# Performance work log

Measured on AMD Instinct MI355X. Metric: run time of the kernel, lower is better.

The kernel has to match this reference:

```python
import jax, jax.numpy as jnp
import numpy as np

B, T, C = 8, 1024, 1024
EPS = 1e-5
NEG_INF = -1e38


def layernorm(x, w, b):
    mu = jnp.mean(x, axis=-1, keepdims=True)
    var = jnp.var(x, axis=-1, keepdims=True)
    return (x - mu) * jax.lax.rsqrt(var + EPS) * w + b


def wkv_scan(w, u, k, v):
    """Numerically-stable RWKV-4 WKV recurrence (forward direction).
    w: [C] (negative decay), u: [C] bonus, k, v: [B, T, C]. Returns [B, T, C]."""
    kt = jnp.swapaxes(k, 0, 1)  # [T, B, C]
    vt = jnp.swapaxes(v, 0, 1)
    bsz = k.shape[0]
    a0 = jnp.zeros((bsz, C), k.dtype)
    b0 = jnp.zeros((bsz, C), k.dtype)
    p0 = jnp.full((bsz, C), NEG_INF, k.dtype)

    def step(carry, inp):
        a, b, p = carry
        kk, vv = inp
        # output at current step (with bonus u on current token)
        q = jnp.maximum(p, u + kk)
        e1 = jnp.exp(p - q)
        e2 = jnp.exp(u + kk - q)
        out = (e1 * a + e2 * vv) / (e1 * b + e2)
        # decay state and absorb current token
        q2 = jnp.maximum(p + w, kk)
        f1 = jnp.exp(p + w - q2)
        f2 = jnp.exp(kk - q2)
        return (f1 * a + f2 * vv, f1 * b + f2, q2), out

    _, outs = jax.lax.scan(step, (a0, b0, p0), (kt, vt))
    return jnp.swapaxes(outs, 0, 1)  # [B, T, C]


def setup_inputs() -> dict:
    key = jax.random.key(0)
    ks = jax.random.split(key, 12)
    s = 0.02
    d = {}
    d["x"] = jax.random.normal(ks[0], (B, T, C), jnp.float32)
    d["ln1_w"] = jnp.ones((C,), jnp.float32)
    d["ln1_b"] = jnp.zeros((C,), jnp.float32)
    d["ln2_w"] = jnp.ones((C,), jnp.float32)
    d["ln2_b"] = jnp.zeros((C,), jnp.float32)
    d["Wr"] = jax.random.normal(ks[1], (C, C), jnp.float32) * s
    d["Wk"] = jax.random.normal(ks[2], (C, C), jnp.float32) * s
    d["Wv"] = jax.random.normal(ks[3], (C, C), jnp.float32) * s
    d["Wo"] = jax.random.normal(ks[4], (C, C), jnp.float32) * s
    d["decay"] = jax.random.normal(ks[5], (C,), jnp.float32) * 0.1
    d["u"] = jax.random.normal(ks[6], (C,), jnp.float32) * 0.1
    d["Wfk"] = jax.random.normal(ks[7], (4 * C, C), jnp.float32) * s
    d["Wfv"] = jax.random.normal(ks[8], (C, 4 * C), jnp.float32) * s
    d["Wfr"] = jax.random.normal(ks[9], (C, C), jnp.float32) * s
    return d


def reference(x, ln1_w, ln1_b, ln2_w, ln2_b, Wr, Wk, Wv, Wo, decay, u, Wfk, Wfv, Wfr):
    # --- bidirectional time-mix (WKV attention) ---
    xn = layernorm(x, ln1_w, ln1_b)
    r = jax.nn.sigmoid(xn @ Wr.T)
    k = xn @ Wk.T
    v = xn @ Wv.T
    w = -jnp.exp(decay)  # per-channel negative decay
    wkv_f = wkv_scan(w, u, k, v)
    wkv_b = jnp.flip(wkv_scan(w, u, jnp.flip(k, axis=1), jnp.flip(v, axis=1)), axis=1)
    wkv = 0.5 * (wkv_f + wkv_b)
    x = x + (r * wkv) @ Wo.T
    # --- channel-mix FFN ---
    xn2 = layernorm(x, ln2_w, ln2_b)
    kk = jnp.square(jax.nn.relu(xn2 @ Wfk.T))  # [B, T, 4C]
    x = x + jax.nn.sigmoid(xn2 @ Wfr.T) * (kk @ Wfv.T)
    return x
```

## Files before the change

### kernel.cpp

```cpp
#include <hip/hip_runtime.h>
#include <cstdint>
#include <cstddef>

typedef unsigned short u16;
typedef __bf16 bf16_t;
typedef bf16_t bf16x8 __attribute__((ext_vector_type(8)));
typedef float f32x4 __attribute__((ext_vector_type(4)));

#define GCH 16
#define TCH 64

static __device__ __forceinline__ float bf2f(u16 v) {
    union { unsigned int u; float f; } cv;
    cv.u = ((unsigned int)v) << 16;
    return cv.f;
}
static __device__ __forceinline__ u16 f2bf(float f) {
    union { float f; unsigned int u; } cv;
    cv.f = f;
    unsigned int r = 0x7fffu + ((cv.u >> 16) & 1u);
    return (u16)((cv.u + r) >> 16);
}

__global__ __launch_bounds__(256)
void f2bf_kernel(const float* __restrict__ in, u16* __restrict__ out, int n4)
{
    const int i = blockIdx.x * 256 + threadIdx.x;
    if (i < n4) {
        float4 f = ((const float4*)in)[i];
        ushort4 o;
        o.x = f2bf(f.x); o.y = f2bf(f.y); o.z = f2bf(f.z); o.w = f2bf(f.w);
        ((ushort4*)out)[i] = o;
    }
}

__global__ __launch_bounds__(256)
void ln_kernel(const float* __restrict__ xin, const float* __restrict__ w,
               const float* __restrict__ b, u16* __restrict__ out)
{
    const int row = blockIdx.x;
    const int tid = threadIdx.x;
    const float4 f = ((const float4*)(xin + (size_t)row * 1024))[tid];
    float vals[4] = { f.x, f.y, f.z, f.w };
    float s  = vals[0] + vals[1] + vals[2] + vals[3];
    float ss = vals[0]*vals[0] + vals[1]*vals[1] + vals[2]*vals[2] + vals[3]*vals[3];
    for (int off = 32; off; off >>= 1) {
        s  += __shfl_down(s, off, 64);
        ss += __shfl_down(ss, off, 64);
    }
    __shared__ float redS[4], redQ[4];
    if ((tid & 63) == 0) { redS[tid >> 6] = s; redQ[tid >> 6] = ss; }
    __syncthreads();
    s  = redS[0] + redS[1] + redS[2] + redS[3];
    ss = redQ[0] + redQ[1] + redQ[2] + redQ[3];
    const float mu  = s * (1.f / 1024.f);
    const float var = ss * (1.f / 1024.f) - mu * mu;
    const float rs  = rsqrtf(var + 1e-5f);
    const float4 wv = ((const float4*)w)[tid];
    const float4 bv = ((const float4*)b)[tid];
    ushort4 o;
    o.x = f2bf((vals[0] - mu) * rs * wv.x + bv.x);
    o.y = f2bf((vals[1] - mu) * rs * wv.y + bv.y);
    o.z = f2bf((vals[2] - mu) * rs * wv.z + bv.z);
    o.w = f2bf((vals[3] - mu) * rs * wv.w + bv.w);
    ((ushort4*)(out + (size_t)row * 1024))[tid] = o;
}

template<int EPI>
__global__ __launch_bounds__(256)
void gemm_bt(const u16* __restrict__ A, const u16* __restrict__ B,
             int M, int N, int K,
             void* __restrict__ outp,
             const void* __restrict__ aux1, const void* __restrict__ aux2)
{
    __shared__ u16 lA[128 * 64];
    __shared__ u16 lB[128 * 64];
    const int tid  = threadIdx.x;
    const int wave = tid >> 6;
    const int lane = tid & 63;
    const int q    = lane >> 4;
    const int l16  = lane & 15;
    const long mBase = (long)blockIdx.x * 128;
    const long nBase = (long)blockIdx.y * 128;
    const int wm = (wave >> 1) * 64;
    const int wn = (wave & 1) * 64;

    f32x4 acc[4][4];
#pragma unroll
    for (int i = 0; i < 4; ++i)
#pragma unroll
        for (int j = 0; j < 4; ++j)
#pragma unroll
            for (int r = 0; r < 4; ++r) acc[i][j][r] = 0.f;

    const int srow = tid >> 3;
    const int scol = ((tid & 7) ^ (srow & 7)) * 8;
    const int ldsW = wave * 512;
    const int swz = l16 & 7;

    for (int kb = 0; kb < K; kb += 64) {
        __syncthreads();
#pragma unroll
        for (int c = 0; c < 4; ++c) {
            const int row = c * 32 + srow;
            const u16* ga = A + (mBase + row) * (long)K + kb + scol;
            const u16* gb = B + (nBase + row) * (long)K + kb + scol;
            __builtin_amdgcn_global_load_lds(
                (const __attribute__((address_space(1))) void*)ga,
                (__attribute__((address_space(3))) void*)(lA + c * 2048 + ldsW),
                16, 0, 0);
            __builtin_amdgcn_global_load_lds(
                (const __attribute__((address_space(1))) void*)gb,
                (__attribute__((address_space(3))) void*)(lB + c * 2048 + ldsW),
                16, 0, 0);
        }
        __syncthreads();
#pragma unroll
        for (int ks = 0; ks < 2; ++ks) {
            const int grp = ((ks * 4 + q) ^ swz) * 8;
            bf16x8 af[4], bfm[4];
#pragma unroll
            for (int i = 0; i < 4; ++i) {
                af[i]  = *(const bf16x8*)(lA + (wm + i * 16 + l16) * 64 + grp);
                bfm[i] = *(const bf16x8*)(lB + (wn + i * 16 + l16) * 64 + grp);
            }
#pragma unroll
            for (int i = 0; i < 4; ++i)
#pragma unroll
                for (int j = 0; j < 4; ++j)
                    acc[i][j] = __builtin_amdgcn_mfma_f32_16x16x32_bf16(
                        af[i], bfm[j], acc[i][j], 0, 0, 0);
        }
    }

    if (EPI == 5 || EPI == 6) {
        u16* optr; long sN, cb;
        if (EPI == 5) {
            const long seg = nBase >> 10;
            optr = (u16*)(seg == 0 ? outp
                        : seg == 1 ? (void*)aux1 : (void*)aux2);
            sN = 1024; cb = (nBase & 1023) + wn + l16;
        } else {
            if (nBase < 4096) { optr = (u16*)outp; sN = 4096; cb = nBase + wn + l16; }
            else { optr = (u16*)aux1; sN = 1024; cb = (nBase - 4096) + wn + l16; }
        }
#pragma unroll
        for (int i = 0; i < 4; ++i)
#pragma unroll
            for (int r = 0; r < 4; ++r) {
                const long row = mBase + wm + i * 16 + q * 4 + r;
                const long rowOff = row * sN + cb;
#pragma unroll
                for (int j = 0; j < 4; ++j) {
                    const float val = acc[i][j][r];
                    float t;
                    if (EPI == 5) t = val;
                    else if (nBase < 4096) t = val > 0.f ? val * val : 0.f;
                    else t = __fdividef(1.f, 1.f + __expf(-val));
                    optr[rowOff + j * 16] = f2bf(t);
                }
            }
    } else {
        const long colBase = nBase + wn + l16;
#pragma unroll
        for (int i = 0; i < 4; ++i) {
#pragma unroll
            for (int r = 0; r < 4; ++r) {
                const long row = mBase + wm + i * 16 + q * 4 + r;
                const long rowOff = row * (long)N;
#pragma unroll
                for (int j = 0; j < 4; ++j) {
                    const long idx = rowOff + colBase + j * 16;
                    const float val = acc[i][j][r];
                    if (EPI == 0) {
                        ((u16*)outp)[idx] = f2bf(val);
                    } else if (EPI == 1) {
                        ((float*)outp)[idx] = ((const float*)aux1)[idx] + val;
                    } else if (EPI == 2) {
                        const float t = val > 0.f ? val * val : 0.f;
                        ((u16*)outp)[idx] = f2bf(t);
                    } else if (EPI == 3) {
                        const float sg = __fdividef(1.f, 1.f + __expf(-val));
                        ((u16*)outp)[idx] = f2bf(sg);
                    } else {
                        const float t = ((const float*)aux1)[idx]
                                      + bf2f(((const u16*)aux2)[idx]) * val;
                        ((float*)outp)[idx] = t;
                    }
                }
            }
        }
    }
}

__global__ __launch_bounds__(64)
void wkv_sum(const u16* __restrict__ kbuf, const u16* __restrict__ vbuf,
             const float* __restrict__ decay,
             float* __restrict__ sumA, float* __restrict__ sumB,
             float* __restrict__ sumP)
{
    const int c   = blockIdx.x * 64 + threadIdx.x;
    const int bt  = blockIdx.y;
    const int dir = blockIdx.z & 1;
    const int g   = blockIdx.z >> 1;
    const long base = (long)bt * (1024 * 1024) + c;
    const long stride = dir ? -1024 : 1024;
    long idx = dir ? base + (long)(1023 - g * TCH) * 1024
                   : base + (long)(g * TCH) * 1024;
    const float w = -__expf(decay[c]);
    float a = 0.f, b = 0.f, p = -1e38f;

    float kq[8], vq[8];
#pragma unroll
    for (int j = 0; j < 8; ++j) {
        kq[j] = bf2f(kbuf[idx + j * stride]);
        vq[j] = bf2f(vbuf[idx + j * stride]);
    }
    for (int tb = 0; tb < TCH / 8; ++tb) {
        float kn[8], vn[8];
        if (tb < TCH / 8 - 1) {
#pragma unroll
            for (int j = 0; j < 8; ++j) {
                kn[j] = bf2f(kbuf[idx + (j + 8) * stride]);
                vn[j] = bf2f(vbuf[idx + (j + 8) * stride]);
            }
        }
#pragma unroll
        for (int j = 0; j < 8; ++j) {
            const float kk = kq[j], vv = vq[j];
            const float pw = p + w;
            const float q2 = fmaxf(pw, kk);
            const float f1 = __expf(pw - q2);
            const float f2 = __expf(kk - q2);
            a = f1 * a + f2 * vv;
            b = f1 * b + f2;
            p = q2;
        }
#pragma unroll
        for (int j = 0; j < 8; ++j) { kq[j] = kn[j]; vq[j] = vn[j]; }
        idx += 8 * stride;
    }
    const int sidx = (((dir * GCH + g) * 8 + bt) << 10) + c;
    sumA[sidx] = a; sumB[sidx] = b; sumP[sidx] = p;
}

__global__ __launch_bounds__(64)
void wkv_out(const u16* __restrict__ kbuf, const u16* __restrict__ vbuf,
             const float* __restrict__ decay, const float* __restrict__ uarr,
             const float* __restrict__ sumA, const float* __restrict__ sumB,
             const float* __restrict__ sumP,
             u16* __restrict__ wkvf, u16* __restrict__ wkvb)
{
    const int c   = blockIdx.x * 64 + threadIdx.x;
    const int bt  = blockIdx.y;
    const int dir = blockIdx.z & 1;
    const int g   = blockIdx.z >> 1;
    const long base = (long)bt * (1024 * 1024) + c;
    const long stride = dir ? -1024 : 1024;
    long idx = dir ? base + (long)(1023 - g * TCH) * 1024
                   : base + (long)(g * TCH) * 1024;
    u16* __restrict__ dst = dir ? wkvb : wkvf;

    const float w  = -__expf(decay[c]);
    const float uu = uarr[c];
    float a = 0.f, b = 0.f, p = -1e38f;
    for (int gg = 0; gg < g; ++gg) {
        const int sidx = (((dir * GCH + gg) * 8 + bt) << 10) + c;
        const float a2 = sumA[sidx], b2 = sumB[sidx], p2 = sumP[sidx];
        const float pd = p + w * (float)TCH;
        const float qq = fmaxf(pd, p2);
        const float x1 = __expf(pd - qq);
        const float x2 = __expf(p2 - qq);
        a = x1 * a + x2 * a2;
        b = x1 * b + x2 * b2;
        p = qq;
    }

    float kq[8], vq[8];
#pragma unroll
    for (int j = 0; j < 8; ++j) {
        kq[j] = bf2f(kbuf[idx + j * stride]);
        vq[j] = bf2f(vbuf[idx + j * stride]);
    }
    for (int tb = 0; tb < TCH / 8; ++tb) {
        float kn[8], vn[8];
        if (tb < TCH / 8 - 1) {
#pragma unroll
            for (int j = 0; j < 8; ++j) {
                kn[j] = bf2f(kbuf[idx + (j + 8) * stride]);
                vn[j] = bf2f(vbuf[idx + (j + 8) * stride]);
            }
        }
#pragma unroll
        for (int j = 0; j < 8; ++j) {
            const float kk = kq[j], vv = vq[j];
            const float uk = uu + kk;
            const float q1 = fmaxf(p, uk);
            const float e1 = __expf(p - q1);
            const float e2 = __expf(uk - q1);
            dst[idx + j * stride] = f2bf(__fdividef(e1 * a + e2 * vv, e1 * b + e2));
            const float pw = p + w;
            const float q2 = fmaxf(pw, kk);
            const float f1 = __expf(pw - q2);
            const float f2 = __expf(kk - q2);
            a = f1 * a + f2 * vv;
            b = f1 * b + f2;
            p = q2;
        }
#pragma unroll
        for (int j = 0; j < 8; ++j) { kq[j] = kn[j]; vq[j] = vn[j]; }
        idx += 8 * stride;
    }
}

__global__ __launch_bounds__(256)
void combine_kernel(u16* __restrict__ wkvf, const u16* __restrict__ wkvb,
                    const u16* __restrict__ rpre)
{
    const int i = blockIdx.x * 256 + threadIdx.x;
    ushort4 fv = ((const ushort4*)wkvf)[i];
    ushort4 bv = ((const ushort4*)wkvb)[i];
    ushort4 rv = ((const ushort4*)rpre)[i];
    ushort4 o;
    {
        float r0 = __fdividef(1.f, 1.f + __expf(-bf2f(rv.x)));
        float r1 = __fdividef(1.f, 1.f + __expf(-bf2f(rv.y)));
        float r2 = __fdividef(1.f, 1.f + __expf(-bf2f(rv.z)));
        float r3 = __fdividef(1.f, 1.f + __expf(-bf2f(rv.w)));
        o.x = f2bf(r0 * 0.5f * (bf2f(fv.x) + bf2f(bv.x)));
        o.y = f2bf(r1 * 0.5f * (bf2f(fv.y) + bf2f(bv.y)));
        o.z = f2bf(r2 * 0.5f * (bf2f(fv.z) + bf2f(bv.z)));
        o.w = f2bf(r3 * 0.5f * (bf2f(fv.w) + bf2f(bv.w)));
    }
    ((ushort4*)wkvf)[i] = o;
}

extern "C" void kernel_launch(void* const* d_in, const int* in_sizes, int n_in,
                              void* d_out, int out_size, void* d_ws, size_t ws_size,
                              hipStream_t stream)
{
    (void)in_sizes; (void)n_in; (void)out_size; (void)ws_size;
    const float* x     = (const float*)d_in[0];
    const float* ln1w  = (const float*)d_in[1];
    const float* ln1b  = (const float*)d_in[2];
    const float* ln2w  = (const float*)d_in[3];
    const float* ln2b  = (const float*)d_in[4];
    const float* Wr    = (const float*)d_in[5];
    const float* Wk    = (const float*)d_in[6];
    const float* Wv    = (const float*)d_in[7];
    const float* Wo    = (const float*)d_in[8];
    const float* decay = (const float*)d_in[9];
    const float* uarr  = (const float*)d_in[10];
    const float* Wfk   = (const float*)d_in[11];
    const float* Wfv   = (const float*)d_in[12];
    const float* Wfr   = (const float*)d_in[13];

    const int M = 8192, C = 1024, C4 = 4096;
    const size_t MB = 1024u * 1024u;
    char* ws = (char*)d_ws;
    float* X2   = (float*)(ws);
    u16*  XN    = (u16*)(ws + 32 * MB);
    u16*  RP    = (u16*)(ws + 48 * MB);
    u16*  KB    = (u16*)(ws + 64 * MB);
    u16*  VB    = (u16*)(ws + 80 * MB);
    u16*  WKVF  = (u16*)(ws + 96 * MB);
    u16*  WKVB  = (u16*)(ws + 112 * MB);
    u16*  KK    = (u16*)(ws + 64 * MB);
    u16*  WrB   = (u16*)(ws + 128 * MB);
    u16*  WkB   = (u16*)(ws + 130 * MB);
    u16*  WvB   = (u16*)(ws + 132 * MB);
    u16*  WoB   = (u16*)(ws + 134 * MB);
    u16*  WfkB  = (u16*)(ws + 136 * MB);
    u16*  WfrB  = (u16*)(ws + 144 * MB);
    u16*  WfvB  = (u16*)(ws + 146 * MB);
    float* sumA = (float*)(ws);
    float* sumB = (float*)(ws + 4 * MB);
    float* sumP = (float*)(ws + 8 * MB);

    const dim3 blk(256);
    const int n4_1M = C * C / 4, n4_4M = C * C4 / 4;

    f2bf_kernel<<<dim3(n4_1M / 256), blk, 0, stream>>>(Wr,  WrB,  n4_1M);
    f2bf_kernel<<<dim3(n4_1M / 256), blk, 0, stream>>>(Wk,  WkB,  n4_1M);
    f2bf_kernel<<<dim3(n4_1M / 256), blk, 0, stream>>>(Wv,  WvB,  n4_1M);
    f2bf_kernel<<<dim3(n4_1M / 256), blk, 0, stream>>>(Wo,  WoB,  n4_1M);
    f2bf_kernel<<<dim3(n4_4M / 256), blk, 0, stream>>>(Wfk, WfkB, n4_4M);
    f2bf_kernel<<<dim3(n4_1M / 256), blk, 0, stream>>>(Wfr, WfrB, n4_1M);
    f2bf_kernel<<<dim3(n4_4M / 256), blk, 0, stream>>>(Wfv, WfvB, n4_4M);

    ln_kernel<<<dim3(M), blk, 0, stream>>>(x, ln1w, ln1b, XN);
    gemm_bt<5><<<dim3(M / 128, 3 * C / 128), blk, 0, stream>>>(
        XN, WrB, M, 3 * C, C, RP, KB, VB);
    wkv_sum<<<dim3(16, 8, 2 * GCH), dim3(64), 0, stream>>>(KB, VB, decay,
                                                           sumA, sumB, sumP);
    wkv_out<<<dim3(16, 8, 2 * GCH), dim3(64), 0, stream>>>(KB, VB, decay, uarr,
                                                           sumA, sumB, sumP,
                                                           WKVF, WKVB);
    combine_kernel<<<dim3(M * C / 4 / 256), blk, 0, stream>>>(WKVF, WKVB, RP);
    gemm_bt<1><<<dim3(M / 128, C / 128), blk, 0, stream>>>(
        WKVF, WoB, M, C, C, X2, x, nullptr);
    ln_kernel<<<dim3(M), blk, 0, stream>>>(X2, ln2w, ln2b, XN);
    gemm_bt<6><<<dim3(M / 128, 5 * C / 128), blk, 0, stream>>>(
        XN, WfkB, M, 5 * C, C, KK, RP, nullptr);
    gemm_bt<4><<<dim3(M / 128, C / 128), blk, 0, stream>>>(
        KK, WfvB, M, C, C4, d_out, X2, RP);
}
```

Before: 488.9 us.

## Fuse bidirectional WKV output with gating, batch weight casts, store residual in bf16

Merges the forward and backward WKV output passes and the sigmoid-gated combine into one kernel, with forward results staged in shared memory. The seven weight-conversion launches become a single batched launch. The intermediate residual X2 is stored as bf16, and each recurrence step uses one exp via the abs-difference trick. This removes intermediate WKV buffers and launches, at the cost of halving WKV grid parallelism and lowering residual precision.

New measurement: 462.1 us. 1.06x faster.

```diff
diff --git a/kernel.cpp b/kernel.cpp
--- a/kernel.cpp
+++ b/kernel.cpp
@@ -22,26 +22,37 @@
     return (u16)((cv.u + r) >> 16);
 }
 
+struct F2BFSegs { const float* src[7]; u16* dst[7]; int n4[7]; };
+
 __global__ __launch_bounds__(256)
-void f2bf_kernel(const float* __restrict__ in, u16* __restrict__ out, int n4)
-{
+void f2bf_all(F2BFSegs s)
+{
+    const int seg = blockIdx.y;
     const int i = blockIdx.x * 256 + threadIdx.x;
-    if (i < n4) {
-        float4 f = ((const float4*)in)[i];
+    if (i < s.n4[seg]) {
+        float4 f = ((const float4*)s.src[seg])[i];
         ushort4 o;
         o.x = f2bf(f.x); o.y = f2bf(f.y); o.z = f2bf(f.z); o.w = f2bf(f.w);
-        ((ushort4*)out)[i] = o;
-    }
-}
-
+        ((ushort4*)s.dst[seg])[i] = o;
+    }
+}
+
+template<int BF16IN>
 __global__ __launch_bounds__(256)
-void ln_kernel(const float* __restrict__ xin, const float* __restrict__ w,
+void ln_kernel(const void* __restrict__ xin, const float* __restrict__ w,
                const float* __restrict__ b, u16* __restrict__ out)
 {
     const int row = blockIdx.x;
     const int tid = threadIdx.x;
-    const float4 f = ((const float4*)(xin + (size_t)row * 1024))[tid];
-    float vals[4] = { f.x, f.y, f.z, f.w };
+    float vals[4];
+    if (BF16IN) {
+        const ushort4 uv = ((const ushort4*)((const u16*)xin + (size_t)row * 1024))[tid];
+        vals[0] = bf2f(uv.x); vals[1] = bf2f(uv.y);
+        vals[2] = bf2f(uv.z); vals[3] = bf2f(uv.w);
+    } else {
+        const float4 f = ((const float4*)((const float*)xin + (size_t)row * 1024))[tid];
+        vals[0] = f.x; vals[1] = f.y; vals[2] = f.z; vals[3] = f.w;
+    }
     float s  = vals[0] + vals[1] + vals[2] + vals[3];
     float ss = vals[0]*vals[0] + vals[1]*vals[1] + vals[2]*vals[2] + vals[3]*vals[3];
     for (int off = 32; off; off >>= 1) {
@@ -172,18 +183,10 @@
                 for (int j = 0; j < 4; ++j) {
                     const long idx = rowOff + colBase + j * 16;
                     const float val = acc[i][j][r];
-                    if (EPI == 0) {
-                        ((u16*)outp)[idx] = f2bf(val);
-                    } else if (EPI == 1) {
-                        ((float*)outp)[idx] = ((const float*)aux1)[idx] + val;
-                    } else if (EPI == 2) {
-                        const float t = val > 0.f ? val * val : 0.f;
-                        ((u16*)outp)[idx] = f2bf(t);
-                    } else if (EPI == 3) {
-                        const float sg = __fdividef(1.f, 1.f + __expf(-val));
-                        ((u16*)outp)[idx] = f2bf(sg);
+                    if (EPI == 1) {
+                        ((u16*)outp)[idx] = f2bf(((const float*)aux1)[idx] + val);
                     } else {
-                        const float t = ((const float*)aux1)[idx]
+                        const float t = bf2f(((const u16*)aux1)[idx])
                                       + bf2f(((const u16*)aux2)[idx]) * val;
                         ((float*)outp)[idx] = t;
                     }
@@ -229,12 +232,13 @@
         for (int j = 0; j < 8; ++j) {
             const float kk = kq[j], vv = vq[j];
             const float pw = p + w;
-            const float q2 = fmaxf(pw, kk);
-            const float f1 = __expf(pw - q2);
-            const float f2 = __expf(kk - q2);
+            const float d  = pw - kk;
+            const float e  = __expf(-fabsf(d));
+            const float f1 = d >= 0.f ? 1.f : e;
+            const float f2 = d >= 0.f ? e : 1.f;
             a = f1 * a + f2 * vv;
             b = f1 * b + f2;
-            p = q2;
+            p = fmaxf(pw, kk);
         }
 #pragma unroll
         for (int j = 0; j < 8; ++j) { kq[j] = kn[j]; vq[j] = vn[j]; }
@@ -245,94 +249,137 @@
 }
 
 __global__ __launch_bounds__(64)
-void wkv_out(const u16* __restrict__ kbuf, const u16* __restrict__ vbuf,
-             const float* __restrict__ decay, const float* __restrict__ uarr,
-             const float* __restrict__ sumA, const float* __restrict__ sumB,
-             const float* __restrict__ sumP,
-             u16* __restrict__ wkvf, u16* __restrict__ wkvb)
-{
-    const int c   = blockIdx.x * 64 + threadIdx.x;
+void wkv_out2(const u16* __restrict__ kbuf, const u16* __restrict__ vbuf,
+              const float* __restrict__ decay, const float* __restrict__ uarr,
+              const float* __restrict__ sumA, const float* __restrict__ sumB,
+              const float* __restrict__ sumP,
+              const u16* __restrict__ rpre, u16* __restrict__ rwkv)
+{
+    __shared__ float fbuf[TCH * 64];
+    const int lane = threadIdx.x;
+    const int c   = blockIdx.x * 64 + lane;
     const int bt  = blockIdx.y;
-    const int dir = blockIdx.z & 1;
-    const int g   = blockIdx.z >> 1;
+    const int g   = blockIdx.z;
     const long base = (long)bt * (1024 * 1024) + c;
-    const long stride = dir ? -1024 : 1024;
-    long idx = dir ? base + (long)(1023 - g * TCH) * 1024
-                   : base + (long)(g * TCH) * 1024;
-    u16* __restrict__ dst = dir ? wkvb : wkvf;
-
+    const long rowBase = base + (long)(g * TCH) * 1024;
     const float w  = -__expf(decay[c]);
     const float uu = uarr[c];
-    float a = 0.f, b = 0.f, p = -1e38f;
-    for (int gg = 0; gg < g; ++gg) {
-        const int sidx = (((dir * GCH + gg) * 8 + bt) << 10) + c;
-        const float a2 = sumA[sidx], b2 = sumB[sidx], p2 = sumP[sidx];
-        const float pd = p + w * (float)TCH;
-        const float qq = fmaxf(pd, p2);
-        const float x1 = __expf(pd - qq);
-        const float x2 = __expf(p2 - qq);
-        a = x1 * a + x2 * a2;
-        b = x1 * b + x2 * b2;
-        p = qq;
-    }
-
-    float kq[8], vq[8];
-#pragma unroll
-    for (int j = 0; j < 8; ++j) {
-        kq[j] = bf2f(kbuf[idx + j * stride]);
-        vq[j] = bf2f(vbuf[idx + j * stride]);
-    }
-    for (int tb = 0; tb < TCH / 8; ++tb) {
-        float kn[8], vn[8];
-        if (tb < TCH / 8 - 1) {
+
+    {
+        float a = 0.f, b = 0.f, p = -1e38f;
+        for (int gg = 0; gg < g; ++gg) {
+            const int sidx = ((gg * 8 + bt) << 10) + c;
+            const float a2 = sumA[sidx], b2 = sumB[sidx], p2 = sumP[sidx];
+            const float pd = p + w * (float)TCH;
+            const float d  = pd - p2;
+            const float e  = __expf(-fabsf(d));
+            const float x1 = d >= 0.f ? 1.f : e;
+            const float x2 = d >= 0.f ? e : 1.f;
+            a = x1 * a + x2 * a2;
+            b = x1 * b + x2 * b2;
+            p = fmaxf(pd, p2);
+        }
+        long idx = rowBase;
+        float kq[8], vq[8];
+#pragma unroll
+        for (int j = 0; j < 8; ++j) {
+            kq[j] = bf2f(kbuf[idx + j * 1024]);
+            vq[j] = bf2f(vbuf[idx + j * 1024]);
+        }
+        for (int tb = 0; tb < TCH / 8; ++tb) {
+            float kn[8], vn[8];
+            if (tb < TCH / 8 - 1) {
+#pragma unroll
+                for (int j = 0; j < 8; ++j) {
+                    kn[j] = bf2f(kbuf[idx + (j + 8) * 1024]);
+                    vn[j] = bf2f(vbuf[idx + (j + 8) * 1024]);
+                }
+            }
 #pragma unroll
             for (int j = 0; j < 8; ++j) {
-                kn[j] = bf2f(kbuf[idx + (j + 8) * stride]);
-                vn[j] = bf2f(vbuf[idx + (j + 8) * stride]);
-            }
-        }
+                const float kk = kq[j], vv = vq[j];
+                const float uk = uu + kk;
+                const float d1 = p - uk;
+                const float e  = __expf(-fabsf(d1));
+                const float e1 = d1 >= 0.f ? 1.f : e;
+                const float e2 = d1 >= 0.f ? e : 1.f;
+                fbuf[(tb * 8 + j) * 64 + lane] =
+                    __fdividef(e1 * a + e2 * vv, e1 * b + e2);
+                const float pw = p + w;
+                const float d2 = pw - kk;
+                const float e_ = __expf(-fabsf(d2));
+                const float f1 = d2 >= 0.f ? 1.f : e_;
+                const float f2 = d2 >= 0.f ? e_ : 1.f;
+                a = f1 * a + f2 * vv;
+                b = f1 * b + f2;
+                p = fmaxf(pw, kk);
+            }
+#pragma unroll
+            for (int j = 0; j < 8; ++j) { kq[j] = kn[j]; vq[j] = vn[j]; }
+            idx += 8 * 1024;
+        }
+    }
+    __syncthreads();
+
+    {
+        float a = 0.f, b = 0.f, p = -1e38f;
+        const int gb = GCH - 1 - g;
+        for (int gg = 0; gg < gb; ++gg) {
+            const int sidx = (((GCH + gg) * 8 + bt) << 10) + c;
+            const float a2 = sumA[sidx], b2 = sumB[sidx], p2 = sumP[sidx];
+            const float pd = p + w * (float)TCH;
+            const float d  = pd - p2;
+            const float e  = __expf(-fabsf(d));
+            const float x1 = d >= 0.f ? 1.f : e;
+            const float x2 = d >= 0.f ? e : 1.f;
+            a = x1 * a + x2 * a2;
+            b = x1 * b + x2 * b2;
+            p = fmaxf(pd, p2);
+        }
+        long idx = rowBase + (long)(TCH - 1) * 1024;
+        float kq[8], vq[8];
 #pragma unroll
         for (int j = 0; j < 8; ++j) {
-            const float kk = kq[j], vv = vq[j];
-            const float uk = uu + kk;
-            const float q1 = fmaxf(p, uk);
-            const float e1 = __expf(p - q1);
-            const float e2 = __expf(uk - q1);
-            dst[idx + j * stride] = f2bf(__fdividef(e1 * a + e2 * vv, e1 * b + e2));
-            const float pw = p + w;
-            const float q2 = fmaxf(pw, kk);
-            const float f1 = __expf(pw - q2);
-            const float f2 = __expf(kk - q2);
-            a = f1 * a + f2 * vv;
-            b = f1 * b + f2;
-            p = q2;
-        }
-#pragma unroll
-        for (int j = 0; j < 8; ++j) { kq[j] = kn[j]; vq[j] = vn[j]; }
-        idx += 8 * stride;
-    }
-}
-
-__global__ __launch_bounds__(256)
-void combine_kernel(u16* __restrict__ wkvf, const u16* __restrict__ wkvb,
-                    const u16* __restrict__ rpre)
-{
-    const int i = blockIdx.x * 256 + threadIdx.x;
-    ushort4 fv = ((const ushort4*)wkvf)[i];
-    ushort4 bv = ((const ushort4*)wkvb)[i];
-    ushort4 rv = ((const ushort4*)rpre)[i];
-    ushort4 o;
-    {
-        float r0 = __fdividef(1.f, 1.f + __expf(-bf2f(rv.x)));
-        float r1 = __fdividef(1.f, 1.f + __expf(-bf2f(rv.y)));
-        float r2 = __fdividef(1.f, 1.f + __expf(-bf2f(rv.z)));
-        float r3 = __fdividef(1.f, 1.f + __expf(-bf2f(rv.w)));
-        o.x = f2bf(r0 * 0.5f * (bf2f(fv.x) + bf2f(bv.x)));
-        o.y = f2bf(r1 * 0.5f * (bf2f(fv.y) + bf2f(bv.y)));
-        o.z = f2bf(r2 * 0.5f * (bf2f(fv.z) + bf2f(bv.z)));
-        o.w = f2bf(r3 * 0.5f * (bf2f(fv.w) + bf2f(bv.w)));
-    }
-    ((ushort4*)wkvf)[i] = o;
+            kq[j] = bf2f(kbuf[idx - j * 1024]);
+            vq[j] = bf2f(vbuf[idx - j * 1024]);
+        }
+        for (int tb = 0; tb < TCH / 8; ++tb) {
+            float kn[8], vn[8];
+            if (tb < TCH / 8 - 1) {
+#pragma unroll
+                for (int j = 0; j < 8; ++j) {
+                    kn[j] = bf2f(kbuf[idx - (j + 8) * 1024]);
+                    vn[j] = bf2f(vbuf[idx - (j + 8) * 1024]);
+                }
+            }
+#pragma unroll
+            for (int j = 0; j < 8; ++j) {
+                const long ii = idx - (long)j * 1024;
+                const int  tl = TCH - 1 - (tb * 8 + j);
+                const float kk = kq[j], vv = vq[j];
+                const float uk = uu + kk;
+                const float d1 = p - uk;
+                const float e  = __expf(-fabsf(d1));
+                const float e1 = d1 >= 0.f ? 1.f : e;
+                const float e2 = d1 >= 0.f ? e : 1.f;
+                const float ob = __fdividef(e1 * a + e2 * vv, e1 * b + e2);
+                const float of = fbuf[tl * 64 + lane];
+                const float rr = __fdividef(1.f, 1.f + __expf(-bf2f(rpre[ii])));
+                rwkv[ii] = f2bf(rr * 0.5f * (of + ob));
+                const float pw = p + w;
+                const float d2 = pw - kk;
+                const float e_ = __expf(-fabsf(d2));
+                const float f1 = d2 >= 0.f ? 1.f : e_;
+                const float f2 = d2 >= 0.f ? e_ : 1.f;
+                a = f1 * a + f2 * vv;
+                b = f1 * b + f2;
+                p = fmaxf(pw, kk);
+            }
+#pragma unroll
+            for (int j = 0; j < 8; ++j) { kq[j] = kn[j]; vq[j] = vn[j]; }
+            idx -= 8 * 1024;
+        }
+    }
 }
 
 extern "C" void kernel_launch(void* const* d_in, const int* in_sizes, int n_in,
@@ -358,48 +405,48 @@
     const int M = 8192, C = 1024, C4 = 4096;
     const size_t MB = 1024u * 1024u;
     char* ws = (char*)d_ws;
-    float* X2   = (float*)(ws);
-    u16*  XN    = (u16*)(ws + 32 * MB);
-    u16*  RP    = (u16*)(ws + 48 * MB);
-    u16*  KB    = (u16*)(ws + 64 * MB);
-    u16*  VB    = (u16*)(ws + 80 * MB);
-    u16*  WKVF  = (u16*)(ws + 96 * MB);
-    u16*  WKVB  = (u16*)(ws + 112 * MB);
-    u16*  KK    = (u16*)(ws + 64 * MB);
-    u16*  WrB   = (u16*)(ws + 128 * MB);
-    u16*  WkB   = (u16*)(ws + 130 * MB);
-    u16*  WvB   = (u16*)(ws + 132 * MB);
-    u16*  WoB   = (u16*)(ws + 134 * MB);
-    u16*  WfkB  = (u16*)(ws + 136 * MB);
-    u16*  WfrB  = (u16*)(ws + 144 * MB);
-    u16*  WfvB  = (u16*)(ws + 146 * MB);
-    float* sumA = (float*)(ws);
-    float* sumB = (float*)(ws + 4 * MB);
-    float* sumP = (float*)(ws + 8 * MB);
+    u16*  X2    = (u16*)(ws);
+    u16*  XN    = (u16*)(ws + 16 * MB);
+    u16*  RP    = (u16*)(ws + 32 * MB);
+    u16*  KB    = (u16*)(ws + 48 * MB);
+    u16*  VB    = (u16*)(ws + 64 * MB);
+    u16*  RWKV  = (u16*)(ws + 80 * MB);
+    u16*  KK    = (u16*)(ws + 48 * MB);
+    float* sumA = (float*)(ws + 112 * MB);
+    float* sumB = (float*)(ws + 113 * MB);
+    float* sumP = (float*)(ws + 114 * MB);
+    u16*  WrB   = (u16*)(ws + 116 * MB);
+    u16*  WkB   = (u16*)(ws + 118 * MB);
+    u16*  WvB   = (u16*)(ws + 120 * MB);
+    u16*  WoB   = (u16*)(ws + 122 * MB);
+    u16*  WfkB  = (u16*)(ws + 124 * MB);
+    u16*  WfrB  = (u16*)(ws + 132 * MB);
+    u16*  WfvB  = (u16*)(ws + 134 * MB);
 
     const dim3 blk(256);
     const int n4_1M = C * C / 4, n4_4M = C * C4 / 4;
 
-    f2bf_kernel<<<dim3(n4_1M / 256), blk, 0, stream>>>(Wr,  WrB,  n4_1M);
-    f2bf_kernel<<<dim3(n4_1M / 256), blk, 0, stream>>>(Wk,  WkB,  n4_1M);
-    f2bf_kernel<<<dim3(n4_1M / 256), blk, 0, stream>>>(Wv,  WvB,  n4_1M);
-    f2bf_kernel<<<dim3(n4_1M / 256), blk, 0, stream>>>(Wo,  WoB,  n4_1M);
-    f2bf_kernel<<<dim3(n4_4M / 256), blk, 0, stream>>>(Wfk, WfkB, n4_4M);
-    f2bf_kernel<<<dim3(n4_1M / 256), blk, 0, stream>>>(Wfr, WfrB, n4_1M);
-    f2bf_kernel<<<dim3(n4_4M / 256), blk, 0, stream>>>(Wfv, WfvB, n4_4M);
-
-    ln_kernel<<<dim3(M), blk, 0, stream>>>(x, ln1w, ln1b, XN);
+    F2BFSegs segs;
+    segs.src[0] = Wr;  segs.dst[0] = WrB;  segs.n4[0] = n4_1M;
+    segs.src[1] = Wk;  segs.dst[1] = WkB;  segs.n4[1] = n4_1M;
+    segs.src[2] = Wv;  segs.dst[2] = WvB;  segs.n4[2] = n4_1M;
+    segs.src[3] = Wo;  segs.dst[3] = WoB;  segs.n4[3] = n4_1M;
+    segs.src[4] = Wfk; segs.dst[4] = WfkB; segs.n4[4] = n4_4M;
+    segs.src[5] = Wfr; segs.dst[5] = WfrB; segs.n4[5] = n4_1M;
+    segs.src[6] = Wfv; segs.dst[6] = WfvB; segs.n4[6] = n4_4M;
+    f2bf_all<<<dim3(n4_4M / 256, 7), blk, 0, stream>>>(segs);
+
+    ln_kernel<0><<<dim3(M), blk, 0, stream>>>(x, ln1w, ln1b, XN);
     gemm_bt<5><<<dim3(M / 128, 3 * C / 128), blk, 0, stream>>>(
         XN, WrB, M, 3 * C, C, RP, KB, VB);
     wkv_sum<<<dim3(16, 8, 2 * GCH), dim3(64), 0, stream>>>(KB, VB, decay,
                                                            sumA, sumB, sumP);
-    wkv_out<<<dim3(16, 8, 2 * GCH), dim3(64), 0, stream>>>(KB, VB, decay, uarr,
-                                                           sumA, sumB, sumP,
-                                                           WKVF, WKVB);
-    combine_kernel<<<dim3(M * C / 4 / 256), blk, 0, stream>>>(WKVF, WKVB, RP);
+    wkv_out2<<<dim3(16, 8, GCH), dim3(64), 0, stream>>>(KB, VB, decay, uarr,
+                                                        sumA, sumB, sumP,
+                                                        RP, RWKV);
     gemm_bt<1><<<dim3(M / 128, C / 128), blk, 0, stream>>>(
-        WKVF, WoB, M, C, C, X2, x, nullptr);
-    ln_kernel<<<dim3(M), blk, 0, stream>>>(X2, ln2w, ln2b, XN);
+        RWKV, WoB, M, C, C, X2, x, nullptr);
+    ln_kernel<1><<<dim3(M), blk, 0, stream>>>(X2, ln2w, ln2b, XN);
     gemm_bt<6><<<dim3(M / 128, 5 * C / 128), blk, 0, stream>>>(
         XN, WfkB, M, 5 * C, C, KK, RP, nullptr);
     gemm_bt<4><<<dim3(M / 128, C / 128), blk, 0, stream>>>(
```
